# Kernel tuning notes

Measured on AMD Instinct MI355X. Metric: run time of the kernel, lower is better.

Reference implementation:

```python
import jax, jax.numpy as jnp
import numpy as np

B, S, D, H = 2, 2048, 1024, 16
DK = D // H  # 64


def rotate_half(x):
    d = x.shape[-1]
    x1, x2 = x[..., : d // 2], x[..., d // 2 :]
    return jnp.concatenate([-x2, x1], axis=-1)


def apply_rope(q, k):
    # q, k: [B, H, S, DK]
    d_k = q.shape[-1]
    seq_len = q.shape[-2]
    theta = 10000.0 ** (-2.0 / d_k * jnp.arange(d_k // 2, dtype=q.dtype))
    positions = jnp.arange(seq_len, dtype=q.dtype)
    angles = jnp.outer(positions, theta)                    # [S, DK/2]
    cos = jnp.tile(jnp.cos(angles), (1, 2))                 # [S, DK]
    sin = jnp.tile(jnp.sin(angles), (1, 2))
    q = q * cos + rotate_half(q) * sin
    k = k * cos + rotate_half(k) * sin
    return q, k


def setup_inputs() -> dict:
    key = jax.random.key(0)
    ks = jax.random.split(key, 9)
    std = 1.0 / np.sqrt(D)
    x = jax.random.normal(ks[0], (B, S, D), dtype=jnp.float32)
    # mask True = masked (code uses masked_fill(mask, -inf)); causal mask
    mask = jnp.triu(jnp.ones((S, S), dtype=bool), k=1)[None, None, :, :]
    mask = jnp.broadcast_to(mask, (B, 1, S, S))
    Wq = jax.random.uniform(ks[1], (D, D), jnp.float32, -std, std)
    bq = jax.random.uniform(ks[2], (D,), jnp.float32, -std, std)
    Wk = jax.random.uniform(ks[3], (D, D), jnp.float32, -std, std)
    bk = jax.random.uniform(ks[4], (D,), jnp.float32, -std, std)
    Wv = jax.random.uniform(ks[5], (D, D), jnp.float32, -std, std)
    bv = jax.random.uniform(ks[6], (D,), jnp.float32, -std, std)
    Wo = jax.random.uniform(ks[7], (D, D), jnp.float32, -std, std)
    bo = jax.random.uniform(ks[8], (D,), jnp.float32, -std, std)
    return {"x": x, "mask": mask, "Wq": Wq, "bq": bq, "Wk": Wk, "bk": bk,
            "Wv": Wv, "bv": bv, "Wo": Wo, "bo": bo}


def reference(x, mask, Wq, bq, Wk, bk, Wv, bv, Wo, bo):
    b, s, d = x.shape
    # projections -> [B, H, S, DK]
    q = (x @ Wq + bq).reshape(b, s, H, DK).transpose(0, 2, 1, 3)
    k = (x @ Wk + bk).reshape(b, s, H, DK).transpose(0, 2, 1, 3)
    v = (x @ Wv + bv).reshape(b, s, H, DK).transpose(0, 2, 1, 3)
    q, k = apply_rope(q, k)
    scores = jnp.einsum("bhqd,bhkd->bhqk", q, k) / np.sqrt(DK)
    scores = jnp.where(mask, -jnp.inf, scores)
    probs = jax.nn.softmax(scores, axis=-1)
    attn = jnp.einsum("bhqk,bhkd->bhqd", probs, v)
    o = attn.transpose(0, 2, 1, 3).reshape(b, s, H * DK)
    return o @ Wo + bo
```

## Files before the change

kernel.cpp:

```cpp
#include <hip/hip_runtime.h>
#include <hip/hip_bf16.h>
#include <math.h>

typedef __hip_bfloat16 bf16;
typedef __attribute__((ext_vector_type(8))) short short8;
typedef __attribute__((ext_vector_type(4))) short s16x4;
typedef __attribute__((ext_vector_type(4))) float f32x4;

#define B_  2
#define S_  2048
#define D_  1024
#define H_  16
#define DK_ 64

#define QSCALE 0.18033688011112043f
#define EXPOFF 11.541560327111707f

__device__ inline short bfs(float f) { return __builtin_bit_cast(short, __float2bfloat16(f)); }

#define GLL16(gptr, lptr)                                                        \
    __builtin_amdgcn_global_load_lds(                                            \
        (const __attribute__((address_space(1))) void*)(gptr),                   \
        (__attribute__((address_space(3))) void*)(lptr), 16, 0, 0)

#if __has_builtin(__builtin_amdgcn_mfma_f32_16x16x16bf16_1k)
#define MFMA_16x16x16(A, Bv, C) __builtin_amdgcn_mfma_f32_16x16x16bf16_1k(A, Bv, C, 0, 0, 0)
#elif __has_builtin(__builtin_amdgcn_mfma_f32_16x16x16_bf16)
#define MFMA_16x16x16(A, Bv, C) __builtin_amdgcn_mfma_f32_16x16x16_bf16(A, Bv, C, 0, 0, 0)
#else
static __device__ inline f32x4 mfma16_asm(s16x4 a, s16x4 b, f32x4 c) {
    f32x4 d;
    asm volatile("v_mfma_f32_16x16x16_bf16 %0, %1, %2, %3\n\ts_nop 7\n\ts_nop 7"
                 : "=v"(d) : "v"(a), "v"(b), "v"(c));
    return d;
}
#define MFMA_16x16x16(A, Bv, C) mfma16_asm(A, Bv, C)
#endif

__global__ __launch_bounds__(256)
void prep_k(const float* __restrict__ x,
            const float* __restrict__ W0, const float* __restrict__ W1,
            const float* __restrict__ W2, const float* __restrict__ W3,
            bf16* __restrict__ cx, bf16* __restrict__ Wt,
            float2* __restrict__ rope)
{
    const int z = blockIdx.z;
    const int t = threadIdx.x;
    if (z == 4) {
        const int bid = blockIdx.y * 16 + blockIdx.x;
        #pragma unroll
        for (int i = 0; i < 16; i++) {
            const size_t g = ((size_t)bid * 256 + t) * 4 + (size_t)i * 262144;
            const float4 v = *(const float4*)(x + g);
            s16x4 o = { bfs(v.x), bfs(v.y), bfs(v.z), bfs(v.w) };
            *(s16x4*)(cx + g) = o;
        }
        return;
    }
    if (z == 5) {
        const int bid = blockIdx.y * 16 + blockIdx.x;
        const int idx = bid * 256 + t;
        const int s = idx >> 5, dk = idx & 31;
        const float th = exp2f((float)dk * -0.41524101186092029f);
        float sn, cs;
        sincosf((float)s * th, &sn, &cs);
        rope[idx] = make_float2(cs, sn);
        return;
    }
    __shared__ float Lt[64][65];
    const float* W = (z == 0) ? W0 : (z == 1) ? W1 : (z == 2) ? W2 : W3;
    bf16* dst = Wt + (size_t)z * D_ * D_;
    const int k0 = blockIdx.y * 64, n0 = blockIdx.x * 64;
    #pragma unroll
    for (int p = 0; p < 4; p++) {
        const int idx = p * 256 + t;
        const int row = idx >> 4, cb = (idx & 15) * 4;
        const float4 v = *(const float4*)(W + (size_t)(k0 + row) * D_ + n0 + cb);
        Lt[cb + 0][row] = v.x; Lt[cb + 1][row] = v.y;
        Lt[cb + 2][row] = v.z; Lt[cb + 3][row] = v.w;
    }
    __syncthreads();
    #pragma unroll
    for (int p = 0; p < 4; p++) {
        const int idx = p * 256 + t;
        const int n = idx >> 4, kb = (idx & 15) * 4;
        s16x4 o = { bfs(Lt[n][kb]), bfs(Lt[n][kb + 1]), bfs(Lt[n][kb + 2]), bfs(Lt[n][kb + 3]) };
        *(s16x4*)(dst + (size_t)(n0 + n) * D_ + k0 + kb) = o;
    }
}

__global__ __launch_bounds__(256)
void gemm_qkv(const bf16* __restrict__ A, const bf16* __restrict__ WtAll,
              const float* __restrict__ b0, const float* __restrict__ b1,
              const float* __restrict__ b2, const float2* __restrict__ rope,
              bf16* __restrict__ d0, bf16* __restrict__ d1, bf16* __restrict__ d2)
{
    constexpr int K = D_;
    const int L = (int)blockIdx.x;
    const int m0 = (L & 31) * 128;
    const int rest = L >> 5;
    const int z = rest >> 4;
    const int n0 = (rest & 15) * 64;
    const bf16* W = WtAll + (size_t)z * D_ * D_;
    const float* bias = (z == 0) ? b0 : (z == 1) ? b1 : b2;

    __shared__ __align__(16) short As[128 * 64];
    __shared__ __align__(16) short Bs[64 * 64];

    const int t = threadIdx.x;
    const int wave = t >> 6, lane = t & 63, quad = lane >> 4, l16 = lane & 15;
    const int wm = wave * 32;

    const int srow  = t >> 3;
    const int sslot = (t & 7) ^ (srow & 7);
    const bf16* gA = A + (size_t)(m0 + srow) * K + sslot * 8;
    const bf16* gW = W + (size_t)(n0 + srow) * K + sslot * 8;
    const int wb = wave * 512;

    f32x4 acc[2][4] = {};

    for (int k0 = 0; k0 < K; k0 += 64) {
        __syncthreads();
        GLL16(gA + k0,                  &As[wb]);
        GLL16(gA + k0 + (size_t)32 * K, &As[2048 + wb]);
        GLL16(gA + k0 + (size_t)64 * K, &As[4096 + wb]);
        GLL16(gA + k0 + (size_t)96 * K, &As[6144 + wb]);
        GLL16(gW + k0,                  &Bs[wb]);
        GLL16(gW + k0 + (size_t)32 * K, &Bs[2048 + wb]);
        __syncthreads();

        const int swz = l16 & 7;
        #pragma unroll
        for (int c = 0; c < 2; c++) {
            const int slot = ((c * 4 + quad) ^ swz) * 8;
            short8 af[2], bfv[4];
            #pragma unroll
            for (int i = 0; i < 2; i++) af[i] = *(const short8*)&As[(wm + i * 16 + l16) * 64 + slot];
            #pragma unroll
            for (int j = 0; j < 4; j++) bfv[j] = *(const short8*)&Bs[(j * 16 + l16) * 64 + slot];
            #pragma unroll
            for (int i = 0; i < 2; i++)
                #pragma unroll
                for (int j = 0; j < 4; j++)
                    acc[i][j] = __builtin_amdgcn_mfma_f32_16x16x32_bf16(af[i], bfv[j], acc[i][j], 0, 0, 0);
        }
    }

    if (z == 2) {
        const int h = n0 >> 6;
        #pragma unroll
        for (int j = 0; j < 4; j++) {
            const int ncol = n0 + j * 16 + l16;
            const float bb = bias[ncol];
            const int dk = ncol & 63;
            #pragma unroll
            for (int i = 0; i < 2; i++) {
                const int mbase = m0 + wm + i * 16 + quad * 4;
                #pragma unroll
                for (int r = 0; r < 4; r++) {
                    const int m = mbase + r;
                    const int b = m >> 11, s = m & (S_ - 1);
                    d2[(((size_t)(b * H_ + h)) * DK_ + dk) * S_ + s] = __float2bfloat16(acc[i][j][r] + bb);
                }
            }
        }
    } else {
        bf16* dst = z ? d1 : d0;
        const float sc = z ? 1.0f : QSCALE;
        const int h = n0 >> 6;
        #pragma unroll
        for (int j = 0; j < 2; j++) {
            const int dk = j * 16 + l16;
            const float blo = bias[(h << 6) + dk];
            const float bhi = bias[(h << 6) + dk + 32];
            #pragma unroll
            for (int i = 0; i < 2; i++) {
                #pragma unroll
                for (int r = 0; r < 4; r++) {
                    const int m = m0 + wm + i * 16 + quad * 4 + r;
                    const int b = m >> 11, s = m & (S_ - 1);
                    const float2 cc = rope[(s << 5) + dk];
                    const float v1 = acc[i][j][r] + blo;
                    const float v2 = acc[i][j + 2][r] + bhi;
                    bf16* p = dst + (((size_t)(b * H_ + h)) * S_ + s) * DK_;
                    p[dk]      = __float2bfloat16((v1 * cc.x - v2 * cc.y) * sc);
                    p[dk + 32] = __float2bfloat16((v2 * cc.x + v1 * cc.y) * sc);
                }
            }
        }
    }
}

__global__ __launch_bounds__(256)
void gemm_o(const bf16* __restrict__ A, const bf16* __restrict__ Wt3,
            const float* __restrict__ bias, float* __restrict__ fout)
{
    constexpr int K = D_;
    const int L = (int)blockIdx.x;
    const int m0 = (L & 63) * 64;
    const int n0 = (L >> 6) * 64;

    __shared__ __align__(16) short As[64 * 64];
    __shared__ __align__(16) short Bs[64 * 64];

    const int t = threadIdx.x;
    const int wave = t >> 6, lane = t & 63, quad = lane >> 4, l16 = lane & 15;
    const int wm = wave * 16;

    const int srow  = t >> 3;
    const int sslot = (t & 7) ^ (srow & 7);
    const bf16* gA = A   + (size_t)(m0 + srow) * K + sslot * 8;
    const bf16* gW = Wt3 + (size_t)(n0 + srow) * K + sslot * 8;
    const int wb = wave * 512;

    f32x4 acc[4] = {};

    for (int k0 = 0; k0 < K; k0 += 64) {
        __syncthreads();
        GLL16(gA + k0,                  &As[wb]);
        GLL16(gA + k0 + (size_t)32 * K, &As[2048 + wb]);
        GLL16(gW + k0,                  &Bs[wb]);
        GLL16(gW + k0 + (size_t)32 * K, &Bs[2048 + wb]);
        __syncthreads();

        const int swz = l16 & 7;
        short8 af[2], bfv[4][2];
        #pragma unroll
        for (int c = 0; c < 2; c++) {
            af[c] = *(const short8*)&As[(wm + l16) * 64 + ((c * 4 + quad) ^ swz) * 8];
            #pragma unroll
            for (int j = 0; j < 4; j++)
                bfv[j][c] = *(const short8*)&Bs[(j * 16 + l16) * 64 + ((c * 4 + quad) ^ swz) * 8];
        }
        #pragma unroll
        for (int c = 0; c < 2; c++)
            #pragma unroll
            for (int j = 0; j < 4; j++)
                acc[j] = __builtin_amdgcn_mfma_f32_16x16x32_bf16(af[c], bfv[j][c], acc[j], 0, 0, 0);
    }

    #pragma unroll
    for (int j = 0; j < 4; j++) {
        const int ncol = n0 + j * 16 + l16;
        const float bb = bias[ncol];
        const int mbase = m0 + wm + quad * 4;
        #pragma unroll
        for (int r = 0; r < 4; r++)
            fout[(size_t)(mbase + r) * D_ + ncol] = acc[j][r] + bb;
    }
}

template<bool DIAG>
__device__ __forceinline__
void attn_tile(const short* __restrict__ Ks, const short* __restrict__ Vts,
               const short8 qf0, const short8 qf1,
               f32x4* ot, float& l_acc,
               const int wave, const int quad, const int l16)
{
    const int kkmax = DIAG ? wave : 3;
    const int swz = l16 & 7;
    #pragma unroll
    for (int kk = 0; kk <= kkmax; kk++) {
        const short8 kf0 = *(const short8*)&Ks[(kk * 16 + l16) * 64 + (quad ^ swz) * 8];
        const short8 kf1 = *(const short8*)&Ks[(kk * 16 + l16) * 64 + ((4 + quad) ^ swz) * 8];
        f32x4 st = {};
        st = __builtin_amdgcn_mfma_f32_16x16x32_bf16(kf0, qf0, st, 0, 0, 0);
        st = __builtin_amdgcn_mfma_f32_16x16x32_bf16(kf1, qf1, st, 0, 0, 0);

        s16x4 pt;
        float psum = 0.0f;
        #pragma unroll
        for (int r = 0; r < 4; r++) {
            float p;
            if (DIAG) {
                const bool masked = (kk == wave) && (quad * 4 + r > l16);
                p = masked ? 0.0f : exp2f(st[r] - EXPOFF);
            } else {
                p = exp2f(st[r] - EXPOFF);
            }
            psum += p;
            pt[r] = bfs(p);
        }
        l_acc += psum;

        #pragma unroll
        for (int dt = 0; dt < 4; dt++) {
            const s16x4 vf = *(const s16x4*)
                &Vts[(dt * 16 + l16) * 64 + ((2 * kk + (quad >> 1)) ^ swz) * 8 + (quad & 1) * 4];
            ot[dt] = MFMA_16x16x16(vf, pt, ot[dt]);
        }
    }
}

__global__ __launch_bounds__(256)
void attn_k(const bf16* __restrict__ q_ws, const bf16* __restrict__ k_ws,
            const bf16* __restrict__ vt_ws, bf16* __restrict__ attn_ws)
{
    __shared__ __align__(16) short Ks[64 * 64];
    __shared__ __align__(16) short Vts[64 * 64];

    const int bh = (int)blockIdx.x;
    const int by = (int)blockIdx.y;
    const int j8 = by & 7, g = by >> 3;
    const int qt = (g == 0) ? (31 - j8) : (g == 1) ? j8 : (g == 2) ? (23 - j8) : (8 + j8);

    const int t = threadIdx.x;
    const int wave = t >> 6, lane = t & 63, quad = lane >> 4, l16 = lane & 15;
    const bf16* Kb = k_ws + (size_t)bh * S_ * DK_;
    const bf16* Vb = vt_ws + (size_t)bh * DK_ * S_;
    const int b = bh >> 4, h = bh & 15;

    const bf16* Qb = q_ws + ((size_t)bh * S_ + qt * 64 + wave * 16) * DK_;
    const short8 qf0 = *(const short8*)(Qb + (size_t)l16 * DK_ + quad * 8);
    const short8 qf1 = *(const short8*)(Qb + (size_t)l16 * DK_ + 32 + quad * 8);

    const int srl  = lane >> 3;
    const int ssl  = (lane & 7) ^ srl;
    const bf16* gK = Kb + (size_t)(wave * 16 + srl) * DK_ + ssl * 8;
    const bf16* gV = Vb + (size_t)(wave * 16 + srl) * S_ + ssl * 8;
    const int wb = wave * 1024;

    float l_acc = 0.0f;
    f32x4 ot[4] = {};

    for (int kt = 0; kt <= qt; kt++) {
        __syncthreads();
        GLL16(gK + (size_t)(kt * 64) * DK_,       &Ks[wb]);
        GLL16(gK + (size_t)(kt * 64 + 8) * DK_,   &Ks[wb + 512]);
        GLL16(gV + kt * 64,                       &Vts[wb]);
        GLL16(gV + kt * 64 + (size_t)8 * S_,      &Vts[wb + 512]);
        __syncthreads();

        if (kt == qt) attn_tile<true >(Ks, Vts, qf0, qf1, ot, l_acc, wave, quad, l16);
        else          attn_tile<false>(Ks, Vts, qf0, qf1, ot, l_acc, wave, quad, l16);
    }

    l_acc += __shfl_xor(l_acc, 16, 64);
    l_acc += __shfl_xor(l_acc, 32, 64);
    const float inv = 1.0f / l_acc;
    const int srow = qt * 64 + wave * 16 + l16;
    bf16* orow = attn_ws + ((size_t)(b * S_ + srow)) * D_ + h * 64;
    #pragma unroll
    for (int dt = 0; dt < 4; dt++) {
        s16x4 o4 = { bfs(ot[dt][0] * inv), bfs(ot[dt][1] * inv),
                     bfs(ot[dt][2] * inv), bfs(ot[dt][3] * inv) };
        *(s16x4*)(orow + dt * 16 + quad * 4) = o4;
    }
}

extern "C" void kernel_launch(void* const* d_in, const int* in_sizes, int n_in,
                              void* d_out, int out_size, void* d_ws, size_t ws_size,
                              hipStream_t stream)
{
    (void)out_size; (void)ws_size;
    const float* x = nullptr;
    const float* W[4] = {nullptr, nullptr, nullptr, nullptr};
    const float* bias[4] = {nullptr, nullptr, nullptr, nullptr};
    int wi = 0, bi = 0;
    for (int i = 0; i < n_in; i++) {
        const int sz = in_sizes[i];
        if (sz == B_ * S_ * D_ && x == nullptr) x = (const float*)d_in[i];
        else if (sz == D_ * D_ && wi < 4) W[wi++] = (const float*)d_in[i];
        else if (sz == D_ && bi < 4) bias[bi++] = (const float*)d_in[i];
    }

    bf16* ws = (bf16*)d_ws;
    const size_t SEG = (size_t)B_ * S_ * D_;
    bf16* canonX  = ws;
    bf16* Wt      = ws + SEG;
    bf16* k_ws    = ws + 2 * SEG;
    bf16* vt_ws   = ws + 3 * SEG;
    bf16* attn_ws = canonX;
    bf16* q_ws    = (bf16*)d_out;
    float2* rope  = (float2*)((bf16*)d_out + SEG);

    prep_k<<<dim3(16, 16, 6), 256, 0, stream>>>(x, W[0], W[1], W[2], W[3], canonX, Wt, rope);

    gemm_qkv<<<dim3(1536, 1, 1), 256, 0, stream>>>(
        canonX, Wt, bias[0], bias[1], bias[2], rope, q_ws, k_ws, vt_ws);

    attn_k<<<dim3(32, 32), 256, 0, stream>>>(q_ws, k_ws, vt_ws, attn_ws);

    gemm_o<<<dim3(1024, 1, 1), 256, 0, stream>>>(
        attn_ws, Wt + (size_t)3 * D_ * D_, bias[3], (float*)d_out);
}
```

Measured before the change: 211.7 us.

## Double-buffer K/V tiles in attention kernel with async LDS prefetch

Doubles the LDS buffers for K and V^T and issues the global-to-LDS loads for the next key tile before computing the current one. Explicit vmcnt/lgkmcnt waits and raw barriers replace the two __syncthreads per iteration, so load latency can overlap with MFMA work. This doubles LDS use per block, which may reduce occupancy, and relies on correct manual wait counts.

```diff
diff --git a/kernel.cpp b/kernel.cpp
--- a/kernel.cpp
+++ b/kernel.cpp
@@ -296,8 +296,8 @@
 void attn_k(const bf16* __restrict__ q_ws, const bf16* __restrict__ k_ws,
             const bf16* __restrict__ vt_ws, bf16* __restrict__ attn_ws)
 {
-    __shared__ __align__(16) short Ks[64 * 64];
-    __shared__ __align__(16) short Vts[64 * 64];
+    __shared__ __align__(16) short Ks[2][64 * 64];
+    __shared__ __align__(16) short Vts[2][64 * 64];
 
     const int bh = (int)blockIdx.x;
     const int by = (int)blockIdx.y;
@@ -323,16 +323,30 @@
     float l_acc = 0.0f;
     f32x4 ot[4] = {};
 
+    GLL16(gK,                   &Ks[0][wb]);
+    GLL16(gK + (size_t)8 * DK_, &Ks[0][wb + 512]);
+    GLL16(gV,                   &Vts[0][wb]);
+    GLL16(gV + (size_t)8 * S_,  &Vts[0][wb + 512]);
+
     for (int kt = 0; kt <= qt; kt++) {
-        __syncthreads();
-        GLL16(gK + (size_t)(kt * 64) * DK_,       &Ks[wb]);
-        GLL16(gK + (size_t)(kt * 64 + 8) * DK_,   &Ks[wb + 512]);
-        GLL16(gV + kt * 64,                       &Vts[wb]);
-        GLL16(gV + kt * 64 + (size_t)8 * S_,      &Vts[wb + 512]);
-        __syncthreads();
-
-        if (kt == qt) attn_tile<true >(Ks, Vts, qf0, qf1, ot, l_acc, wave, quad, l16);
-        else          attn_tile<false>(Ks, Vts, qf0, qf1, ot, l_acc, wave, quad, l16);
+        const int cur = kt & 1;
+        asm volatile("s_waitcnt lgkmcnt(0)" ::: "memory");
+        __builtin_amdgcn_s_barrier();
+        if (kt < qt) {
+            const int nxt = cur ^ 1;
+            GLL16(gK + (size_t)((kt + 1) * 64) * DK_,       &Ks[nxt][wb]);
+            GLL16(gK + (size_t)((kt + 1) * 64 + 8) * DK_,   &Ks[nxt][wb + 512]);
+            GLL16(gV + (kt + 1) * 64,                       &Vts[nxt][wb]);
+            GLL16(gV + (kt + 1) * 64 + (size_t)8 * S_,      &Vts[nxt][wb + 512]);
+            asm volatile("s_waitcnt vmcnt(4)" ::: "memory");
+        } else {
+            asm volatile("s_waitcnt vmcnt(0)" ::: "memory");
+        }
+        __builtin_amdgcn_s_barrier();
+        __builtin_amdgcn_sched_barrier(0);
+
+        if (kt == qt) attn_tile<true >(Ks[cur], Vts[cur], qf0, qf1, ot, l_acc, wave, quad, l16);
+        else          attn_tile<false>(Ks[cur], Vts[cur], qf0, qf1, ot, l_acc, wave, quad, l16);
     }
 
     l_acc += __shfl_xor(l_acc, 16, 64);
```

Measured after the change: 212.4 us. Within noise of the previous version (+0.3%).
